# Optimization experiments

Hardware: AMD Instinct MI355X
Metric: run time of the kernel (lower is better)

The kernel has to match this reference:

```python
import jax, jax.numpy as jnp
import numpy as np

BATCH, D, F, K_DIM = 8192, 512, 64, 64


def setup_inputs() -> dict:
    key = jax.random.key(0)
    k1, k2, k3 = jax.random.split(key, 3)
    x = jax.random.normal(k1, (BATCH, D), dtype=jnp.float32)
    # glorot-uniform-ish scale for the FFM kernel (D, F, K)
    limit = float(np.sqrt(6.0 / (D + K_DIM)))
    kernel = jax.random.uniform(k2, (D, F, K_DIM), dtype=jnp.float32,
                                minval=-limit, maxval=limit)
    field_dict = jax.random.randint(k3, (D,), 0, F, dtype=jnp.int32)
    return {"x": x, "kernel": kernel, "field_dict": field_dict}


def reference(x, kernel, field_dict):
    # A[i, j, :] = kernel[i, field_dict[j], :]   -> (D, D, K)
    A = kernel[:, field_dict, :]
    # weight[i, j] = <kernel[i, field[j]], kernel[j, field[i]]>
    W = jnp.einsum('ijk,jik->ij', A, A)  # (D, D)
    # keep only pairs i < j, matching the nested-loop accumulation
    mask = jnp.triu(jnp.ones((x.shape[1], x.shape[1]), dtype=x.dtype), k=1)
    Wm = W * mask
    # out[b] = sum_{i<j} W[i,j] * x[b,i] * x[b,j]
    return jnp.einsum('bi,ij,bj->b', x, Wm, x)
```

## Files before the change

kernel.cpp:

```cpp
#include <hip/hip_runtime.h>
#include <hip/hip_bf16.h>

#define BATCH 8192
#define DDIM 512
#define FDIM 64
#define KD 64

typedef __attribute__((ext_vector_type(8))) short short8;
typedef __attribute__((ext_vector_type(4))) float f32x4;

static __device__ __forceinline__ unsigned short f2bf(float f) {
    __hip_bfloat16 h = __float2bfloat16(f);
    return *reinterpret_cast<unsigned short*>(&h);
}

__global__ __launch_bounds__(256) void w_kernel(const float* __restrict__ kern,
                                                const int* __restrict__ fd,
                                                unsigned short* __restrict__ WT,
                                                float* __restrict__ out) {
    const int j = blockIdx.x;
    const int tid = threadIdx.x;

    __shared__ float Bv[FDIM * KD];
    __shared__ int fds[DDIM];

    if (tid < 16) out[j * 16 + tid] = 0.f;

    {
        const float4* src = reinterpret_cast<const float4*>(kern + (size_t)j * FDIM * KD);
        float4* dst = reinterpret_cast<float4*>(Bv);
#pragma unroll
        for (int u = 0; u < 4; ++u) dst[u * 256 + tid] = src[u * 256 + tid];
        fds[tid] = fd[tid];
        fds[tid + 256] = fd[tid + 256];
    }
    __syncthreads();

    const int fdj = fds[j];
    const int g = tid >> 4;
    const int gl = tid & 15;

#pragma unroll 2
    for (int it = 0; it < DDIM / 16; ++it) {
        const int i = it * 16 + g;
        float s = 0.f;
        if (i < j) {
            float4 a = *reinterpret_cast<const float4*>(kern + ((size_t)i * FDIM + fdj) * KD + gl * 4);
            float4 b = *reinterpret_cast<const float4*>(Bv + fds[i] * KD + gl * 4);
            s = a.x * b.x + a.y * b.y + a.z * b.z + a.w * b.w;
        }
#pragma unroll
        for (int off = 1; off < 16; off <<= 1) s += __shfl_xor(s, off);
        if (gl == 0) WT[(size_t)j * DDIM + i] = f2bf(s);
    }
}

#define BM 64
#define BN 128
#define BK 32
#define KSTEPS 4

__global__ __launch_bounds__(256, 4) void quad_kernel(const float* __restrict__ x,
                                                      const unsigned short* __restrict__ WT,
                                                      float* __restrict__ out) {
    __shared__ unsigned short As[BM * BK];
    __shared__ unsigned short Bs[BN * BK];

    const int tid = threadIdx.x;
    const int lane = tid & 63;
    const int w = tid >> 6;
    const int wm = w >> 1, wn = w & 1;
    const int ln = lane & 15, l4 = lane >> 4;

    const int mb = blockIdx.x & 127;
    const int c = blockIdx.x >> 7;
    const int nb = (c >= 1) + (c >= 3) + (c >= 6);
    const int chunk = c - nb * (nb + 1) / 2;
    const int nbase = nb * BN;
    const int mbase = mb * BM;
    const int kbase = chunk * (KSTEPS * BK);

    f32x4 acc[2][4] = {};

    const int arow = tid >> 2, ac = tid & 3;
    const int brow = tid >> 1, bh = tid & 1;

    float4 aA0, aA1, aB0, aB1;
    int4 bA0, bA1, bB0, bB1;

    auto loadT = [&](int kk, float4& a0, float4& a1, int4& b0, int4& b1) {
        const float4* srcA = reinterpret_cast<const float4*>(x + (size_t)(mbase + arow) * DDIM + kk + ac * 8);
        a0 = srcA[0]; a1 = srcA[1];
        const int4* srcB = reinterpret_cast<const int4*>(WT + (size_t)(nbase + brow) * DDIM + kk + bh * 16);
        b0 = srcB[0]; b1 = srcB[1];
    };
    auto writeT = [&](float4& a0, float4& a1, int4& b0, int4& b1) {
        short8 v;
        v[0] = (short)f2bf(a0.x); v[1] = (short)f2bf(a0.y);
        v[2] = (short)f2bf(a0.z); v[3] = (short)f2bf(a0.w);
        v[4] = (short)f2bf(a1.x); v[5] = (short)f2bf(a1.y);
        v[6] = (short)f2bf(a1.z); v[7] = (short)f2bf(a1.w);
        int cs = ac ^ (arow & 3) ^ ((arow >> 2) & 3);
        *reinterpret_cast<short8*>(As + arow * BK + cs * 8) = v;
        int c0 = (bh * 2 + 0) ^ (brow & 3) ^ ((brow >> 2) & 3);
        int c1 = (bh * 2 + 1) ^ (brow & 3) ^ ((brow >> 2) & 3);
        *reinterpret_cast<int4*>(Bs + brow * BK + c0 * 8) = b0;
        *reinterpret_cast<int4*>(Bs + brow * BK + c1 * 8) = b1;
    };
    auto computeT = [&]() {
        short8 a[2], b[4];
#pragma unroll
        for (int m = 0; m < 2; ++m) {
            int row = wm * 32 + m * 16 + ln;
            int ch = l4 ^ (row & 3) ^ ((row >> 2) & 3);
            a[m] = *reinterpret_cast<const short8*>(As + row * BK + ch * 8);
        }
#pragma unroll
        for (int n = 0; n < 4; ++n) {
            int col = wn * 64 + n * 16 + ln;
            int ch = l4 ^ (col & 3) ^ ((col >> 2) & 3);
            b[n] = *reinterpret_cast<const short8*>(Bs + col * BK + ch * 8);
        }
#pragma unroll
        for (int m = 0; m < 2; ++m)
#pragma unroll
            for (int n = 0; n < 4; ++n)
                acc[m][n] = __builtin_amdgcn_mfma_f32_16x16x32_bf16(a[m], b[n], acc[m][n], 0, 0, 0);
    };

    loadT(kbase, aA0, aA1, bA0, bA1);
#pragma unroll
    for (int t = 0; t < KSTEPS; t += 2) {
        if (t + 1 < KSTEPS) loadT(kbase + (t + 1) * BK, aB0, aB1, bB0, bB1);
        __syncthreads();
        writeT(aA0, aA1, bA0, bA1);
        __syncthreads();
        computeT();
        if (t + 2 < KSTEPS) loadT(kbase + (t + 2) * BK, aA0, aA1, bA0, bA1);
        __syncthreads();
        writeT(aB0, aB1, bB0, bB1);
        __syncthreads();
        computeT();
    }

#pragma unroll
    for (int m = 0; m < 2; ++m) {
#pragma unroll
        for (int q = 0; q < 4; ++q) {
            int grow = mbase + wm * 32 + m * 16 + l4 * 4 + q;
            float s = 0.f;
#pragma unroll
            for (int n = 0; n < 4; ++n) {
                int gcol = nbase + wn * 64 + n * 16 + ln;
                s += acc[m][n][q] * x[(size_t)grow * DDIM + gcol];
            }
#pragma unroll
            for (int off = 1; off < 16; off <<= 1)
                s += __shfl_xor(s, off, 64);
            if (ln == 0) atomicAdd(out + grow, s);
        }
    }
}

extern "C" void kernel_launch(void* const* d_in, const int* in_sizes, int n_in,
                              void* d_out, int out_size, void* d_ws, size_t ws_size,
                              hipStream_t stream) {
    const float* x = (const float*)d_in[0];
    const float* kern = (const float*)d_in[1];
    const int* fd = (const int*)d_in[2];
    float* out = (float*)d_out;

    unsigned short* WT = (unsigned short*)d_ws;

    w_kernel<<<DDIM, 256, 0, stream>>>(kern, fd, WT, out);
    quad_kernel<<<1280, 256, 0, stream>>>(x, WT, out);
}
```

Before: 33.46 us.

## Pre-convert x to bf16, split W kernel, stage GEMM tiles via direct global-to-LDS loads

The W kernel now runs on a 4xD grid. Each block also converts a slice of x to bf16 into workspace, and blocks whose i-range lies entirely at or above j just write zeros and exit instead of looping over masked pairs. The quad kernel then loads bf16 x and W tiles straight into double-buffered LDS with global_load_lds, which removes the register round trip, the in-kernel conversion and the XOR swizzle. This is meant to cut the GEMM's load and sync overhead. The cost is an extra bf16 write and read of x, and LDS bank conflicts may appear now that the swizzle is gone.

```diff
diff --git a/kernel.cpp b/kernel.cpp
--- a/kernel.cpp
+++ b/kernel.cpp
@@ -14,18 +14,48 @@
     return *reinterpret_cast<unsigned short*>(&h);
 }
 
+static __device__ __forceinline__ void gll16(const void* g, void* l) {
+    __builtin_amdgcn_global_load_lds(
+        (const __attribute__((address_space(1))) void*)g,
+        (__attribute__((address_space(3))) void*)l, 16, 0, 0);
+}
+
 __global__ __launch_bounds__(256) void w_kernel(const float* __restrict__ kern,
                                                 const int* __restrict__ fd,
+                                                const float* __restrict__ x,
                                                 unsigned short* __restrict__ WT,
+                                                unsigned short* __restrict__ xb,
                                                 float* __restrict__ out) {
-    const int j = blockIdx.x;
+    const int iq = blockIdx.x;
+    const int j = blockIdx.y;
     const int tid = threadIdx.x;
+
+    {
+        const size_t base = ((size_t)j * 4 + iq) * 2048;
+        const float4* X4 = reinterpret_cast<const float4*>(x + base);
+        float4 p = X4[tid * 2];
+        float4 q = X4[tid * 2 + 1];
+        short8 v;
+        v[0] = (short)f2bf(p.x); v[1] = (short)f2bf(p.y);
+        v[2] = (short)f2bf(p.z); v[3] = (short)f2bf(p.w);
+        v[4] = (short)f2bf(q.x); v[5] = (short)f2bf(q.y);
+        v[6] = (short)f2bf(q.z); v[7] = (short)f2bf(q.w);
+        *reinterpret_cast<short8*>(xb + base + tid * 8) = v;
+    }
+
+    if (iq == 0 && tid < 16) out[j * 16 + tid] = 0.f;
+
+    const int ibase = iq * 128;
+    if (ibase >= j) {
+        if (tid < 16) {
+            short8 z = {};
+            *reinterpret_cast<short8*>(WT + (size_t)j * DDIM + ibase + tid * 8) = z;
+        }
+        return;
+    }
 
     __shared__ float Bv[FDIM * KD];
     __shared__ int fds[DDIM];
-
-    if (tid < 16) out[j * 16 + tid] = 0.f;
-
     {
         const float4* src = reinterpret_cast<const float4*>(kern + (size_t)j * FDIM * KD);
         float4* dst = reinterpret_cast<float4*>(Bv);
@@ -40,9 +70,9 @@
     const int g = tid >> 4;
     const int gl = tid & 15;
 
-#pragma unroll 2
-    for (int it = 0; it < DDIM / 16; ++it) {
-        const int i = it * 16 + g;
+#pragma unroll 4
+    for (int it = 0; it < 8; ++it) {
+        const int i = ibase + it * 16 + g;
         float s = 0.f;
         if (i < j) {
             float4 a = *reinterpret_cast<const float4*>(kern + ((size_t)i * FDIM + fdj) * KD + gl * 4);
@@ -60,11 +90,12 @@
 #define BK 32
 #define KSTEPS 4
 
-__global__ __launch_bounds__(256, 4) void quad_kernel(const float* __restrict__ x,
+__global__ __launch_bounds__(256, 4) void quad_kernel(const unsigned short* __restrict__ xb,
                                                       const unsigned short* __restrict__ WT,
+                                                      const float* __restrict__ x,
                                                       float* __restrict__ out) {
-    __shared__ unsigned short As[BM * BK];
-    __shared__ unsigned short Bs[BN * BK];
+    __shared__ unsigned short As[2][BM * BK];
+    __shared__ unsigned short Bs[2][BN * BK];
 
     const int tid = threadIdx.x;
     const int lane = tid & 63;
@@ -82,44 +113,25 @@
 
     f32x4 acc[2][4] = {};
 
-    const int arow = tid >> 2, ac = tid & 3;
-    const int brow = tid >> 1, bh = tid & 1;
+    const int srow = tid >> 2;
+    const int sk = (tid & 3) * 8;
 
-    float4 aA0, aA1, aB0, aB1;
-    int4 bA0, bA1, bB0, bB1;
-
-    auto loadT = [&](int kk, float4& a0, float4& a1, int4& b0, int4& b1) {
-        const float4* srcA = reinterpret_cast<const float4*>(x + (size_t)(mbase + arow) * DDIM + kk + ac * 8);
-        a0 = srcA[0]; a1 = srcA[1];
-        const int4* srcB = reinterpret_cast<const int4*>(WT + (size_t)(nbase + brow) * DDIM + kk + bh * 16);
-        b0 = srcB[0]; b1 = srcB[1];
+    auto stage = [&](int kk, int buf) {
+        gll16(xb + (size_t)(mbase + srow) * DDIM + kk + sk, &As[buf][tid * 8]);
+        gll16(WT + (size_t)(nbase + srow) * DDIM + kk + sk, &Bs[buf][tid * 8]);
+        gll16(WT + (size_t)(nbase + 64 + srow) * DDIM + kk + sk, &Bs[buf][2048 + tid * 8]);
     };
-    auto writeT = [&](float4& a0, float4& a1, int4& b0, int4& b1) {
-        short8 v;
-        v[0] = (short)f2bf(a0.x); v[1] = (short)f2bf(a0.y);
-        v[2] = (short)f2bf(a0.z); v[3] = (short)f2bf(a0.w);
-        v[4] = (short)f2bf(a1.x); v[5] = (short)f2bf(a1.y);
-        v[6] = (short)f2bf(a1.z); v[7] = (short)f2bf(a1.w);
-        int cs = ac ^ (arow & 3) ^ ((arow >> 2) & 3);
-        *reinterpret_cast<short8*>(As + arow * BK + cs * 8) = v;
-        int c0 = (bh * 2 + 0) ^ (brow & 3) ^ ((brow >> 2) & 3);
-        int c1 = (bh * 2 + 1) ^ (brow & 3) ^ ((brow >> 2) & 3);
-        *reinterpret_cast<int4*>(Bs + brow * BK + c0 * 8) = b0;
-        *reinterpret_cast<int4*>(Bs + brow * BK + c1 * 8) = b1;
-    };
-    auto computeT = [&]() {
+    auto compute = [&](int buf) {
         short8 a[2], b[4];
 #pragma unroll
         for (int m = 0; m < 2; ++m) {
             int row = wm * 32 + m * 16 + ln;
-            int ch = l4 ^ (row & 3) ^ ((row >> 2) & 3);
-            a[m] = *reinterpret_cast<const short8*>(As + row * BK + ch * 8);
+            a[m] = *reinterpret_cast<const short8*>(&As[buf][row * BK + l4 * 8]);
         }
 #pragma unroll
         for (int n = 0; n < 4; ++n) {
             int col = wn * 64 + n * 16 + ln;
-            int ch = l4 ^ (col & 3) ^ ((col >> 2) & 3);
-            b[n] = *reinterpret_cast<const short8*>(Bs + col * BK + ch * 8);
+            b[n] = *reinterpret_cast<const short8*>(&Bs[buf][col * BK + l4 * 8]);
         }
 #pragma unroll
         for (int m = 0; m < 2; ++m)
@@ -128,20 +140,18 @@
                 acc[m][n] = __builtin_amdgcn_mfma_f32_16x16x32_bf16(a[m], b[n], acc[m][n], 0, 0, 0);
     };
 
-    loadT(kbase, aA0, aA1, bA0, bA1);
-#pragma unroll
-    for (int t = 0; t < KSTEPS; t += 2) {
-        if (t + 1 < KSTEPS) loadT(kbase + (t + 1) * BK, aB0, aB1, bB0, bB1);
-        __syncthreads();
-        writeT(aA0, aA1, bA0, bA1);
-        __syncthreads();
-        computeT();
-        if (t + 2 < KSTEPS) loadT(kbase + (t + 2) * BK, aA0, aA1, bA0, bA1);
-        __syncthreads();
-        writeT(aB0, aB1, bB0, bB1);
-        __syncthreads();
-        computeT();
-    }
+    stage(kbase, 0);
+    __syncthreads();
+    stage(kbase + BK, 1);
+    compute(0);
+    __syncthreads();
+    stage(kbase + 2 * BK, 0);
+    compute(1);
+    __syncthreads();
+    stage(kbase + 3 * BK, 1);
+    compute(0);
+    __syncthreads();
+    compute(1);
 
 #pragma unroll
     for (int m = 0; m < 2; ++m) {
@@ -171,7 +181,9 @@
     float* out = (float*)d_out;
 
     unsigned short* WT = (unsigned short*)d_ws;
+    unsigned short* xb = WT + (size_t)DDIM * DDIM;
 
-    w_kernel<<<DDIM, 256, 0, stream>>>(kern, fd, WT, out);
-    quad_kernel<<<1280, 256, 0, stream>>>(x, WT, out);
+    dim3 wgrid(4, DDIM);
+    w_kernel<<<wgrid, 256, 0, stream>>>(kern, fd, x, WT, xb, out);
+    quad_kernel<<<1280, 256, 0, stream>>>(xb, WT, x, out);
 }
```

After: 28.34 us. 15.3% less time.
